# Optimization experiments

Measured on AMD Instinct MI355X. Metric: run time of the kernel, lower is better.

## Reference

```python
import jax, jax.numpy as jnp
import numpy as np

EPS = 1.1920929e-7  # torch.finfo(float32).eps, default for F.rms_norm
ATTN_SCALE = 0.1
ROPE_BASE = 10000.0


def _rms_norm(x):
    # F.rms_norm over last dim, no learned weight
    return x * jax.lax.rsqrt(jnp.mean(x * x, axis=-1, keepdims=True) + EPS)


def _rotary(x):
    # x: [B, T, H, D]; rotates halves as in the Rotary module
    T, D = x.shape[1], x.shape[3]
    half = D // 2
    inv_freq = 1.0 / (ROPE_BASE ** (jnp.arange(0, D, 2, dtype=jnp.float32) / D))  # [half]
    freqs = jnp.arange(T, dtype=jnp.float32)[:, None] * inv_freq[None, :]          # [T, half]
    cos = jnp.cos(freqs)[None, :, None, :]
    sin = jnp.sin(freqs)[None, :, None, :]
    x1, x2 = x[..., :half], x[..., half:]
    return jnp.concatenate([x1 * cos + x2 * sin, -x1 * sin + x2 * cos], axis=-1)


def setup_inputs() -> dict:
    key = jax.random.key(0)
    ks = jax.random.split(key, 8)
    B, T, dim, H, hd = 2, 2048, 1024, 16, 64
    gate_in = 12
    s = 1.0 / np.sqrt(dim)
    return {
        "x": jax.random.normal(ks[0], (B, T, dim), dtype=jnp.float32),
        "v1": jax.random.normal(ks[1], (B, T, H, hd), dtype=jnp.float32),
        "Wq": jax.random.uniform(ks[2], (dim, dim), jnp.float32, -s, s),
        "Wk": jax.random.uniform(ks[3], (dim, dim), jnp.float32, -s, s),
        "Wv": jax.random.uniform(ks[4], (dim, dim), jnp.float32, -s, s),
        "Wproj": jax.random.uniform(ks[5], (dim, dim), jnp.float32, -s, s),
        "Wg": jax.random.uniform(ks[6], (H, gate_in), jnp.float32,
                                  -1.0 / np.sqrt(gate_in), 1.0 / np.sqrt(gate_in)),
        "lamb": jnp.float32(0.5),
    }


def reference(x, v1, Wq, Wk, Wv, Wproj, Wg, lamb):
    B, T, dim = x.shape
    H, hd = v1.shape[2], v1.shape[3]
    q = (x @ Wq.T).reshape(B, T, H, hd)
    k = (x @ Wk.T).reshape(B, T, H, hd)
    v = (x @ Wv.T).reshape(B, T, H, hd)
    # value-residual mixing
    v = (1.0 - lamb) * v + lamb * v1
    # QK RMSNorm + RoPE
    q = _rotary(_rms_norm(q))
    k = _rotary(_rms_norm(k))
    # causal SDPA with fixed scale
    scores = jnp.einsum('bqhd,bkhd->bhqk', q, k) * ATTN_SCALE
    causal = jnp.tril(jnp.ones((T, T), dtype=bool))
    scores = jnp.where(causal[None, None], scores, jnp.float32(-jnp.inf))
    probs = jax.nn.softmax(scores, axis=-1)
    y = jnp.einsum('bhqk,bkhd->bqhd', probs, v)  # [B, T, H, hd]
    # sigmoid gate from first 12 channels of x
    gate = jax.nn.sigmoid(x[..., :Wg.shape[1]] @ Wg.T)  # [B, T, H]
    y = y * gate[..., None]
    y = y.reshape(B, T, H * hd) @ Wproj.T
    return y
```

## Files before the change

kernel.cpp:

```cpp
#include <hip/hip_runtime.h>
#include <math.h>


#define B_    2
#define T_    2048
#define DIM_  1024
#define H_    16
#define HD_   64
#define NROW  (B_ * T_)
#define EPS_  1.1920929e-07f
#define SCALE_ 0.1f
#define LOG2_10K 13.287712379549449f
#define INV2PI 0.15915494309189535f

typedef unsigned short u16;
typedef unsigned int   u32;
typedef __bf16 bf16x8 __attribute__((ext_vector_type(8)));
typedef __bf16 bf16x2 __attribute__((ext_vector_type(2)));
typedef float  f32x4  __attribute__((ext_vector_type(4)));

__device__ __forceinline__ u16 f2b(float f) {
  u32 u = __float_as_uint(f);
  u += 0x7fffu + ((u >> 16) & 1u);
  return (u16)(u >> 16);
}
__device__ __forceinline__ u32 pk2(float a, float b) {
#if __has_builtin(__builtin_amdgcn_cvt_pk_bf16_f32)
  bf16x2 r = __builtin_amdgcn_cvt_pk_bf16_f32(a, b);
  return __builtin_bit_cast(u32, r);
#else
  return (u32)f2b(a) | ((u32)f2b(b) << 16);
#endif
}
__device__ __forceinline__ void fast_sincos_rev(float rev, float* s, float* c) {
  const float r = rev - floorf(rev);
#if __has_builtin(__builtin_amdgcn_sinf) && __has_builtin(__builtin_amdgcn_cosf)
  *s = __builtin_amdgcn_sinf(r);
  *c = __builtin_amdgcn_cosf(r);
#else
  *s = __sinf(r * 6.283185307179586f);
  *c = __cosf(r * 6.283185307179586f);
#endif
}
#define MFMA16(a,b,c) __builtin_amdgcn_mfma_f32_16x16x32_bf16((a),(b),(c),0,0,0)

typedef const __attribute__((address_space(1))) unsigned char gbuf_t;
typedef __attribute__((address_space(3))) unsigned char lbuf_t;
__device__ __forceinline__ void gload_lds16(const u16* g, unsigned char* l) {
  __builtin_amdgcn_global_load_lds((gbuf_t*)g, (lbuf_t*)l, 16, 0, 0);
}

__global__ __launch_bounds__(256) void convert_all(
    const float* __restrict__ x, const float* __restrict__ Wq,
    const float* __restrict__ Wk, const float* __restrict__ Wv,
    const float* __restrict__ Wp,
    u16* __restrict__ xb, u16* __restrict__ wb) {
  const int i = blockIdx.x * 256 + threadIdx.x;
  if (i < 1835008) {
    const float* src; u16* dst; int off;
    if (i < 1048576)      { src = x;  dst = xb;           off = i; }
    else if (i < 1310720) { src = Wq; dst = wb;           off = i - 1048576; }
    else if (i < 1572864) { src = Wk; dst = wb + 1048576; off = i - 1310720; }
    else                  { src = Wv; dst = wb + 2097152; off = i - 1572864; }
    const float4 f = ((const float4*)src)[off];
    uint2 o;
    o.x = pk2(f.x, f.y);
    o.y = pk2(f.z, f.w);
    ((uint2*)dst)[off] = o;
  } else {
    const int off = i - 1835008;
    const int blk = off >> 6, ln = off & 63;
    const int row = ((blk >> 5) << 4) + (ln & 15);
    const int col = ((blk & 31) << 5) + ((ln >> 4) << 3);
    const float4 f0 = *(const float4*)(Wp + (size_t)row * DIM_ + col);
    const float4 f1 = *(const float4*)(Wp + (size_t)row * DIM_ + col + 4);
    uint4 o;
    o.x = pk2(f0.x, f0.y); o.y = pk2(f0.z, f0.w);
    o.z = pk2(f1.x, f1.y); o.w = pk2(f1.z, f1.w);
    ((uint4*)(wb + 3145728))[off] = o;
  }
}

__global__ __launch_bounds__(256) void gemm_qkv(
    const u16* __restrict__ Ab, const u16* __restrict__ Wb,
    u16* __restrict__ qo, u16* __restrict__ ko, u16* __restrict__ vto,
    const float* __restrict__ v1, const float* __restrict__ lambp) {
  __shared__ __attribute__((aligned(16))) unsigned char sm[49152];
  const int tid  = threadIdx.x;
  const int w    = tid >> 6;
  const int lane = tid & 63;
  const int lo = lane & 15, hi = lane >> 4;
  const int m0 = blockIdx.x << 7;
  const int by = blockIdx.y;
  const int mode = by >> 3;
  const int n0 = (by & 7) << 7;
  const u16* W = Wb + (size_t)mode * (DIM_ * DIM_);
  const int wm = w & 1, wn = w >> 1;

  const u16* agA0 = Ab + (size_t)(m0 + (2 * w + 0) * 16 + lo) * DIM_ + (hi << 3);
  const u16* agA1 = Ab + (size_t)(m0 + (2 * w + 1) * 16 + lo) * DIM_ + (hi << 3);
  const u16* agB0 = W  + (size_t)(n0 + (2 * w + 0) * 16 + lo) * DIM_ + (hi << 3);
  const u16* agB1 = W  + (size_t)(n0 + (2 * w + 1) * 16 + lo) * DIM_ + (hi << 3);

  f32x4 acc[4][4];
#pragma unroll
  for (int i = 0; i < 4; ++i)
#pragma unroll
    for (int j = 0; j < 4; ++j) acc[i][j] = (f32x4){0.f, 0.f, 0.f, 0.f};

  {
    unsigned char* ad0 = sm + (2 * w) * 1024;
    gload_lds16(agA0, ad0);
    gload_lds16(agA1, ad0 + 1024);
    gload_lds16(agB0, ad0 + 8192);
    gload_lds16(agB1, ad0 + 9216);
    agA0 += 32; agA1 += 32; agB0 += 32; agB1 += 32;
    unsigned char* ad1 = sm + 16384 + (2 * w) * 1024;
    gload_lds16(agA0, ad1);
    gload_lds16(agA1, ad1 + 1024);
    gload_lds16(agB0, ad1 + 8192);
    gload_lds16(agB1, ad1 + 9216);
    agA0 += 32; agA1 += 32; agB0 += 32; agB1 += 32;
  }

  int cr = 0, cw = 2;
  for (int kc = 0; kc < DIM_; kc += 32) {
    __builtin_amdgcn_sched_barrier(0);
    if (kc + 32 < DIM_) {
      asm volatile("s_waitcnt vmcnt(4)" ::: "memory");
    } else {
      asm volatile("s_waitcnt vmcnt(0)" ::: "memory");
    }
    __builtin_amdgcn_s_barrier();
    __builtin_amdgcn_sched_barrier(0);
    if (kc + 64 < DIM_) {
      unsigned char* ad = sm + cw * 16384 + (2 * w) * 1024;
      gload_lds16(agA0, ad);
      gload_lds16(agA1, ad + 1024);
      gload_lds16(agB0, ad + 8192);
      gload_lds16(agB1, ad + 9216);
      agA0 += 32; agA1 += 32; agB0 += 32; agB1 += 32;
    }
    const unsigned char* Acur = sm + cr * 16384;
    const unsigned char* Bcur = Acur + 8192;
    bf16x8 bfr[4];
#pragma unroll
    for (int nt = 0; nt < 4; ++nt)
      bfr[nt] = *(const bf16x8*)(Bcur + (((wn * 4 + nt) * 64 + lane) << 4));
#pragma unroll
    for (int mt = 0; mt < 4; ++mt) {
      const bf16x8 af = *(const bf16x8*)(Acur + (((wm * 4 + mt) * 64 + lane) << 4));
#pragma unroll
      for (int nt = 0; nt < 4; ++nt)
        acc[mt][nt] = MFMA16(af, bfr[nt], acc[mt][nt]);
    }
    cr = (cr == 2) ? 0 : cr + 1;
    cw = (cw == 2) ? 0 : cw + 1;
  }

  const int head = (n0 >> 6) + wn;
  if (mode <= 1) {
    u16* C = (mode == 0) ? qo : ko;
    const float if0 = exp2f(-(float)lo * (LOG2_10K / 32.f)) * INV2PI;
    const float if1 = exp2f(-(float)(lo + 16) * (LOG2_10K / 32.f)) * INV2PI;
#pragma unroll
    for (int mt = 0; mt < 4; ++mt)
#pragma unroll
      for (int r = 0; r < 4; ++r) {
        float ss = 0.f;
#pragma unroll
        for (int nt = 0; nt < 4; ++nt) { const float v = acc[mt][nt][r]; ss += v * v; }
        ss += __shfl_xor(ss, 1, 64); ss += __shfl_xor(ss, 2, 64);
        ss += __shfl_xor(ss, 4, 64); ss += __shfl_xor(ss, 8, 64);
        float scl = rsqrtf(ss * (1.f / 64.f) + EPS_);
        if (mode == 0) scl *= SCALE_;
        const int row_g = m0 + wm * 64 + mt * 16 + hi * 4 + r;
        const float tpos = (float)(row_g & (T_ - 1));
        float sn0, cs0, sn1, cs1;
        fast_sincos_rev(tpos * if0, &sn0, &cs0);
        fast_sincos_rev(tpos * if1, &sn1, &cs1);
        u16* crow = C + (size_t)row_g * DIM_ + head * HD_;
        const float x10 = acc[mt][0][r] * scl, x11 = acc[mt][1][r] * scl;
        const float x20 = acc[mt][2][r] * scl, x21 = acc[mt][3][r] * scl;
        crow[lo]      = f2b(x10 * cs0 + x20 * sn0);
        crow[16 + lo] = f2b(x11 * cs1 + x21 * sn1);
        crow[32 + lo] = f2b(x20 * cs0 - x10 * sn0);
        crow[48 + lo] = f2b(x21 * cs1 - x11 * sn1);
      }
  } else {
    const float lam = lambp[0];
#pragma unroll
    for (int mt = 0; mt < 4; ++mt)
#pragma unroll
      for (int r = 0; r < 4; ++r) {
        const int row_g = m0 + wm * 64 + mt * 16 + hi * 4 + r;
        const int bb = row_g >> 11, tt = row_g & (T_ - 1);
        const int bh = bb * H_ + head;
        const float* v1r = v1 + (size_t)row_g * DIM_ + head * HD_;
#pragma unroll
        for (int nt = 0; nt < 4; ++nt) {
          const int d = nt * 16 + lo;
          const float ov = (1.f - lam) * acc[mt][nt][r] + lam * v1r[d];
          vto[((size_t)(bh * HD_ + d)) * T_ + tt] = f2b(ov);
        }
      }
  }
}

__global__ __launch_bounds__(256) void gemm_proj(
    const u16* __restrict__ Ab, const u16* __restrict__ Wb,
    float* __restrict__ fo) {
  const int tid  = threadIdx.x;
  const int w    = tid >> 6;
  const int lane = tid & 63;
  const int lo = lane & 15, hi = lane >> 4;
  const int raw = blockIdx.x;
  const int xcd = raw & 7;
  const int jj  = raw >> 3;
  const int m0 = (xcd * 4 + (jj & 3)) << 7;
  const int n0 = (jj >> 2) << 7;
  const int wm = w & 1, wn = w >> 1;

  const u16* pA = Ab + (size_t)((m0 >> 4) + wm * 4) * 16384 + lane * 8;
  const u16* pB = Wb + (size_t)((n0 >> 4) + wn * 4) * 16384 + lane * 8;

  f32x4 acc[4][4];
#pragma unroll
  for (int i = 0; i < 4; ++i)
#pragma unroll
    for (int j = 0; j < 4; ++j) acc[i][j] = (f32x4){0.f, 0.f, 0.f, 0.f};

  bf16x8 aE[4], bE[4], aO[4], bO[4];
#pragma unroll
  for (int t = 0; t < 4; ++t) {
    aE[t] = *(const bf16x8*)(pA + t * 16384);
    bE[t] = *(const bf16x8*)(pB + t * 16384);
  }
  for (int ks = 0; ks < 32; ks += 2) {
#pragma unroll
    for (int t = 0; t < 4; ++t) {
      aO[t] = *(const bf16x8*)(pA + t * 16384 + (ks + 1) * 512);
      bO[t] = *(const bf16x8*)(pB + t * 16384 + (ks + 1) * 512);
    }
#pragma unroll
    for (int mt = 0; mt < 4; ++mt)
#pragma unroll
      for (int nt = 0; nt < 4; ++nt)
        acc[mt][nt] = MFMA16(aE[mt], bE[nt], acc[mt][nt]);
    const int kn = (ks + 2 < 32) ? (ks + 2) : 0;
#pragma unroll
    for (int t = 0; t < 4; ++t) {
      aE[t] = *(const bf16x8*)(pA + t * 16384 + kn * 512);
      bE[t] = *(const bf16x8*)(pB + t * 16384 + kn * 512);
    }
#pragma unroll
    for (int mt = 0; mt < 4; ++mt)
#pragma unroll
      for (int nt = 0; nt < 4; ++nt)
        acc[mt][nt] = MFMA16(aO[mt], bO[nt], acc[mt][nt]);
  }

#pragma unroll
  for (int mt = 0; mt < 4; ++mt)
#pragma unroll
    for (int r = 0; r < 4; ++r) {
      const int row_g = m0 + wm * 64 + mt * 16 + hi * 4 + r;
      float* orow = fo + (size_t)row_g * DIM_ + n0 + wn * 64;
#pragma unroll
      for (int nt = 0; nt < 4; ++nt) orow[nt * 16 + lo] = acc[mt][nt][r];
    }
}

__global__ __launch_bounds__(256) void gate_kernel(
    const float* __restrict__ x, const float* __restrict__ Wg,
    float* __restrict__ gate) {
  const int id = blockIdx.x * 256 + threadIdx.x;
  const int n = id >> 4, h = id & 15;
  const float* xr = x + (size_t)n * DIM_;
  const float* wr = Wg + h * 12;
  float s = 0.f;
#pragma unroll
  for (int j = 0; j < 12; ++j) s += xr[j] * wr[j];
  gate[id] = 1.f / (1.f + __expf(-s));
}

__global__ __launch_bounds__(256) void attn3(
    const u16* __restrict__ q, const u16* __restrict__ k, const u16* __restrict__ vt,
    const float* __restrict__ gate, u16* __restrict__ yt) {
  __shared__ __attribute__((aligned(16))) unsigned char smem[49152];
  const int tid = threadIdx.x;
  const int wv = tid >> 6, lane = tid & 63, lo = lane & 15, hi = lane >> 4;
  const int raw = blockIdx.x;
  const int xcd = raw & 7;
  const int jj  = raw >> 3;
  const int qt = 31 - (jj >> 2);
  const int bh = xcd * 4 + (jj & 3);
  const int b = bh >> 4, h = bh & 15;
  const int qb = qt << 6;

  const int qrow = b * T_ + qb + wv * 16 + lo;
  const u16* qp = q + (size_t)qrow * DIM_ + h * HD_;
  const bf16x8 qf0 = *(const bf16x8*)(qp + hi * 8);
  const bf16x8 qf1 = *(const bf16x8*)(qp + 32 + hi * 8);

  f32x4 o[4];
#pragma unroll
  for (int i = 0; i < 4; ++i) o[i] = (f32x4){0.f, 0.f, 0.f, 0.f};
  float lrun = 0.f;

  const int sl = tid & 63, skh = (tid >> 6) & 1, st0 = tid >> 7;
  const int srow = sl & 15, skk = skh * 32 + ((sl >> 4) << 3);
  const u16* kg0 = k + ((size_t)(b * T_ + st0 * 16 + srow)) * DIM_ + h * HD_ + skk;
  const u16* kg1 = kg0 + (size_t)32 * DIM_;
  const u16* vg0 = vt + ((size_t)(bh * HD_ + st0 * 16 + srow)) * T_ + skk;
  const u16* vg1 = vg0 + (size_t)32 * T_;
  const int wub = (tid >> 6) << 10;

  {
    gload_lds16(kg0, smem + wub);
    gload_lds16(kg1, smem + 4096 + wub);
    gload_lds16(vg0, smem + 8192 + wub);
    gload_lds16(vg1, smem + 12288 + wub);
    const int t1 = (qt >= 1) ? 1 : 0;
    const size_t ko = (size_t)t1 * 64 * DIM_;
    const size_t vo = (size_t)t1 * 64;
    unsigned char* b1 = smem + 16384;
    gload_lds16(kg0 + ko, b1 + wub);
    gload_lds16(kg1 + ko, b1 + 4096 + wub);
    gload_lds16(vg0 + vo, b1 + 8192 + wub);
    gload_lds16(vg1 + vo, b1 + 12288 + wub);
  }

  int sr = 0, sw = 2;
  for (int tix = 0; tix <= qt; ++tix) {
    __builtin_amdgcn_sched_barrier(0);
    if (tix < qt) {
      asm volatile("s_waitcnt vmcnt(4)" ::: "memory");
    } else {
      asm volatile("s_waitcnt vmcnt(0)" ::: "memory");
    }
    __builtin_amdgcn_s_barrier();
    __builtin_amdgcn_sched_barrier(0);
    if (tix + 2 <= qt) {
      const size_t ko = (size_t)(tix + 2) * 64 * DIM_;
      const size_t vo = (size_t)(tix + 2) * 64;
      unsigned char* base = smem + sw * 16384;
      gload_lds16(kg0 + ko, base + wub);
      gload_lds16(kg1 + ko, base + 4096 + wub);
      gload_lds16(vg0 + vo, base + 8192 + wub);
      gload_lds16(vg1 + vo, base + 12288 + wub);
    }
    const unsigned char* kb = smem + sr * 16384;
    const unsigned char* vb = kb + 8192;

    f32x4 stl[4];
#pragma unroll
    for (int kt = 0; kt < 4; ++kt) stl[kt] = (f32x4){0.f, 0.f, 0.f, 0.f};
    __builtin_amdgcn_s_setprio(1);
#pragma unroll
    for (int kh = 0; kh < 2; ++kh) {
      const bf16x8 qb_ = kh ? qf1 : qf0;
#pragma unroll
      for (int kt = 0; kt < 4; ++kt) {
        const bf16x8 af = *(const bf16x8*)(kb + (((kt * 2 + kh) * 64 + lane) << 4));
        stl[kt] = MFMA16(af, qb_, stl[kt]);
      }
    }
    __builtin_amdgcn_s_setprio(0);
    float ps = 0.f;
    if (tix != qt) {
#pragma unroll
      for (int kt = 0; kt < 4; ++kt)
#pragma unroll
        for (int r = 0; r < 4; ++r) {
          const float e = __expf(stl[kt][r]);
          stl[kt][r] = e;
          ps += e;
        }
    } else {
#pragma unroll
      for (int kt = 0; kt < 4; ++kt)
#pragma unroll
        for (int r = 0; r < 4; ++r) {
          float s = stl[kt][r];
          if (kt * 16 + hi * 4 + r > wv * 16 + lo) s = -3e38f;
          const float e = __expf(s);
          stl[kt][r] = e;
          ps += e;
        }
    }
    ps += __shfl_xor(ps, 16, 64);
    ps += __shfl_xor(ps, 32, 64);
    lrun += ps;

    u32 pkv[4][2];
#pragma unroll
    for (int kt = 0; kt < 4; ++kt) {
      pkv[kt][0] = pk2(stl[kt][0], stl[kt][1]);
      pkv[kt][1] = pk2(stl[kt][2], stl[kt][3]);
    }
#pragma unroll
    for (int kh = 0; kh < 2; ++kh) {
      uint4 w4;
      u32* w4p = (u32*)&w4;
#pragma unroll
      for (int wd = 0; wd < 4; ++wd) {
        const int src = (2 * (hi & 1) + (wd >> 1)) * 16 + lo;
        const u32 a  = (u32)__shfl((int)pkv[2 * kh][wd & 1], src, 64);
        const u32 bb = (u32)__shfl((int)pkv[2 * kh + 1][wd & 1], src, 64);
        w4p[wd] = (hi < 2) ? a : bb;
      }
      const bf16x8 pf = __builtin_bit_cast(bf16x8, w4);
      __builtin_amdgcn_s_setprio(1);
#pragma unroll
      for (int dt = 0; dt < 4; ++dt) {
        const bf16x8 vf = *(const bf16x8*)(vb + (((dt * 2 + kh) * 64 + lane) << 4));
        o[dt] = MFMA16(vf, pf, o[dt]);
      }
      __builtin_amdgcn_s_setprio(0);
    }
    sr = (sr == 2) ? 0 : sr + 1;
    sw = (sw == 2) ? 0 : sw + 1;
  }

  const float inv = gate[(size_t)qrow * H_ + h] / lrun;
  u16* ybase = yt + (size_t)(qrow >> 4) * 16384 + (size_t)(h * 2) * 512
             + lo * 8 + (hi & 1) * 4;
#pragma unroll
  for (int dt = 0; dt < 4; ++dt) {
    ushort4 pq;
    pq.x = f2b(o[dt][0] * inv); pq.y = f2b(o[dt][1] * inv);
    pq.z = f2b(o[dt][2] * inv); pq.w = f2b(o[dt][3] * inv);
    const int c = (dt * 2 + (hi >> 1)) & 3;
    *(ushort4*)(ybase + (dt >> 1) * 512 + c * 128) = pq;
  }
}

extern "C" void kernel_launch(void* const* d_in, const int* in_sizes, int n_in,
                              void* d_out, int out_size, void* d_ws, size_t ws_size,
                              hipStream_t stream) {
  const float* x    = (const float*)d_in[0];
  const float* v1   = (const float*)d_in[1];
  const float* Wq   = (const float*)d_in[2];
  const float* Wk   = (const float*)d_in[3];
  const float* Wv   = (const float*)d_in[4];
  const float* Wp   = (const float*)d_in[5];
  const float* Wg   = (const float*)d_in[6];
  const float* lamb = (const float*)d_in[7];

  const size_t NX = (size_t)NROW * DIM_;
  const size_t NW = (size_t)DIM_ * DIM_;

  u16* q  = (u16*)d_ws;
  u16* k  = q + NX;
  u16* vt = k + NX;
  u16* xb = vt + NX;
  u16* wb = xb + NX;
  float* gate = (float*)(wb + 4 * NW);

  const dim3 bb(256);

  convert_all<<<dim3(7680), bb, 0, stream>>>(x, Wq, Wk, Wv, Wp, xb, wb);
  gemm_qkv<<<dim3(32, 24), bb, 0, stream>>>(xb, wb, q, k, vt, v1, lamb);
  gate_kernel<<<dim3(NROW * H_ / 256), bb, 0, stream>>>(x, Wg, gate);
  attn3<<<dim3(1024), bb, 0, stream>>>(q, k, vt, gate, xb);
  gemm_proj<<<dim3(256), bb, 0, stream>>>(xb, wb + 3 * NW, (float*)d_out);
}
```

Baseline: 222.1 us.

## Halve proj GEMM N-tile to double grid; move attention scale into softmax

The output projection GEMM now uses 128x64 tiles instead of 128x128 and launches 512 blocks instead of 256. This raises occupancy and gives each CU more waves to hide load latency, at the cost of reloading A tiles twice as often. The attention scale is no longer folded into q at QKV-GEMM time. It is applied to scores in the softmax instead, and the diagonal and non-diagonal exp branches are merged into one loop with a predicate. The scale moves off q's bf16 rounding but adds a multiply per score.

```diff
diff --git a/kernel.cpp b/kernel.cpp
--- a/kernel.cpp
+++ b/kernel.cpp
@@ -172,8 +172,7 @@
         for (int nt = 0; nt < 4; ++nt) { const float v = acc[mt][nt][r]; ss += v * v; }
         ss += __shfl_xor(ss, 1, 64); ss += __shfl_xor(ss, 2, 64);
         ss += __shfl_xor(ss, 4, 64); ss += __shfl_xor(ss, 8, 64);
-        float scl = rsqrtf(ss * (1.f / 64.f) + EPS_);
-        if (mode == 0) scl *= SCALE_;
+        const float scl = rsqrtf(ss * (1.f / 64.f) + EPS_);
         const int row_g = m0 + wm * 64 + mt * 16 + hi * 4 + r;
         const float tpos = (float)(row_g & (T_ - 1));
         float sn0, cs0, sn1, cs1;
@@ -218,45 +217,46 @@
   const int xcd = raw & 7;
   const int jj  = raw >> 3;
   const int m0 = (xcd * 4 + (jj & 3)) << 7;
-  const int n0 = (jj >> 2) << 7;
+  const int n0 = (jj >> 2) << 6;
   const int wm = w & 1, wn = w >> 1;
 
   const u16* pA = Ab + (size_t)((m0 >> 4) + wm * 4) * 16384 + lane * 8;
-  const u16* pB = Wb + (size_t)((n0 >> 4) + wn * 4) * 16384 + lane * 8;
-
-  f32x4 acc[4][4];
+  const u16* pB = Wb + (size_t)((n0 >> 4) + wn * 2) * 16384 + lane * 8;
+
+  f32x4 acc[4][2];
 #pragma unroll
   for (int i = 0; i < 4; ++i)
 #pragma unroll
-    for (int j = 0; j < 4; ++j) acc[i][j] = (f32x4){0.f, 0.f, 0.f, 0.f};
-
-  bf16x8 aE[4], bE[4], aO[4], bO[4];
-#pragma unroll
-  for (int t = 0; t < 4; ++t) {
-    aE[t] = *(const bf16x8*)(pA + t * 16384);
-    bE[t] = *(const bf16x8*)(pB + t * 16384);
-  }
+    for (int j = 0; j < 2; ++j) acc[i][j] = (f32x4){0.f, 0.f, 0.f, 0.f};
+
+  bf16x8 aE[4], bE[2], aO[4], bO[2];
+#pragma unroll
+  for (int t = 0; t < 4; ++t) aE[t] = *(const bf16x8*)(pA + t * 16384);
+#pragma unroll
+  for (int t = 0; t < 2; ++t) bE[t] = *(const bf16x8*)(pB + t * 16384);
   for (int ks = 0; ks < 32; ks += 2) {
 #pragma unroll
-    for (int t = 0; t < 4; ++t) {
+    for (int t = 0; t < 4; ++t)
       aO[t] = *(const bf16x8*)(pA + t * 16384 + (ks + 1) * 512);
+#pragma unroll
+    for (int t = 0; t < 2; ++t)
       bO[t] = *(const bf16x8*)(pB + t * 16384 + (ks + 1) * 512);
-    }
 #pragma unroll
     for (int mt = 0; mt < 4; ++mt)
 #pragma unroll
-      for (int nt = 0; nt < 4; ++nt)
+      for (int nt = 0; nt < 2; ++nt)
         acc[mt][nt] = MFMA16(aE[mt], bE[nt], acc[mt][nt]);
     const int kn = (ks + 2 < 32) ? (ks + 2) : 0;
 #pragma unroll
-    for (int t = 0; t < 4; ++t) {
+    for (int t = 0; t < 4; ++t)
       aE[t] = *(const bf16x8*)(pA + t * 16384 + kn * 512);
+#pragma unroll
+    for (int t = 0; t < 2; ++t)
       bE[t] = *(const bf16x8*)(pB + t * 16384 + kn * 512);
-    }
 #pragma unroll
     for (int mt = 0; mt < 4; ++mt)
 #pragma unroll
-      for (int nt = 0; nt < 4; ++nt)
+      for (int nt = 0; nt < 2; ++nt)
         acc[mt][nt] = MFMA16(aO[mt], bO[nt], acc[mt][nt]);
   }
 
@@ -265,9 +265,9 @@
 #pragma unroll
     for (int r = 0; r < 4; ++r) {
       const int row_g = m0 + wm * 64 + mt * 16 + hi * 4 + r;
-      float* orow = fo + (size_t)row_g * DIM_ + n0 + wn * 64;
-#pragma unroll
-      for (int nt = 0; nt < 4; ++nt) orow[nt * 16 + lo] = acc[mt][nt][r];
+      float* orow = fo + (size_t)row_g * DIM_ + n0 + wn * 32;
+#pragma unroll
+      for (int nt = 0; nt < 2; ++nt) orow[nt * 16 + lo] = acc[mt][nt][r];
     }
 }
 
@@ -367,28 +367,18 @@
       }
     }
     __builtin_amdgcn_s_setprio(0);
+    const bool diag = (tix == qt);
     float ps = 0.f;
-    if (tix != qt) {
-#pragma unroll
-      for (int kt = 0; kt < 4; ++kt)
-#pragma unroll
-        for (int r = 0; r < 4; ++r) {
-          const float e = __expf(stl[kt][r]);
-          stl[kt][r] = e;
-          ps += e;
-        }
-    } else {
-#pragma unroll
-      for (int kt = 0; kt < 4; ++kt)
-#pragma unroll
-        for (int r = 0; r < 4; ++r) {
-          float s = stl[kt][r];
-          if (kt * 16 + hi * 4 + r > wv * 16 + lo) s = -3e38f;
-          const float e = __expf(s);
-          stl[kt][r] = e;
-          ps += e;
-        }
-    }
+#pragma unroll
+    for (int kt = 0; kt < 4; ++kt)
+#pragma unroll
+      for (int r = 0; r < 4; ++r) {
+        float s = stl[kt][r] * SCALE_;
+        if (diag && (kt * 16 + hi * 4 + r > wv * 16 + lo)) s = -3e38f;
+        const float e = __expf(s);
+        stl[kt][r] = e;
+        ps += e;
+      }
     ps += __shfl_xor(ps, 16, 64);
     ps += __shfl_xor(ps, 32, 64);
     lrun += ps;
@@ -464,5 +454,5 @@
   gemm_qkv<<<dim3(32, 24), bb, 0, stream>>>(xb, wb, q, k, vt, v1, lamb);
   gate_kernel<<<dim3(NROW * H_ / 256), bb, 0, stream>>>(x, Wg, gate);
   attn3<<<dim3(1024), bb, 0, stream>>>(q, k, vt, gate, xb);
-  gemm_proj<<<dim3(256), bb, 0, stream>>>(xb, wb + 3 * NW, (float*)d_out);
-}
+  gemm_proj<<<dim3(512), bb, 0, stream>>>(xb, wb + 3 * NW, (float*)d_out);
+}
```

New measurement: 222.8 us. About the same (+0.3%).
